# Kernel tuning notes

Hardware: AMD Instinct MI355X
Metric: run time of the kernel (lower is better)

## Reference

```python
import jax, jax.numpy as jnp
import numpy as np

B, S, H, K, V = 1024, 50, 128, 4, 100000
ROUTING_TIMES = 3

def _squash(c):
    # c: [B,K,1,H]
    cap_norm = jnp.sum(jnp.square(c), -1, keepdims=True)
    scalar_factor = cap_norm / (1.0 + cap_norm) / jnp.sqrt(cap_norm + 1e-9)
    return scalar_factor * c

def setup_inputs() -> dict:
    key = jax.random.key(0)
    k1, k2, k3, k4, k5, k6 = jax.random.split(key, 6)
    item_seq = jax.random.randint(k1, (B, S), 0, V)
    mask = jax.random.randint(k2, (B, S), 0, 2).astype(jnp.float32)
    item = jax.random.randint(k3, (B, 1), 0, V)
    emb = jax.random.normal(k4, (V, H), dtype=jnp.float32) * 0.02
    W = jax.random.normal(k5, (H, H), dtype=jnp.float32) * (1.0 / np.sqrt(H))
    # bilinear_type==0 -> capsule routing logits initialized with randn
    capsule_weight0 = jax.random.normal(k6, (B, K, S), dtype=jnp.float32)
    return {"item_seq": item_seq, "mask": mask, "item": item,
            "emb": emb, "W": W, "capsule_weight0": capsule_weight0}

def reference(item_seq, mask, item, emb, W, capsule_weight0):
    # padding_idx=0: lookups see a zeroed row 0 (and get no grad there),
    # but calculate_loss uses the raw weight matrix.
    emb_lookup = emb.at[0].set(0.0)
    seq_emb = emb_lookup[item_seq]          # [B,S,H]
    item_e = emb_lookup[item[:, 0]]         # [B,H]  (squeeze(1))

    # CapsuleNetwork, bilinear_type==0: Linear(H,H,no bias) then repeat_interleave along hidden
    h = seq_emb @ W.T                        # [B,S,H]
    hat = jnp.repeat(h, K, axis=2)           # [B,S,H*K] (repeat_interleave semantics)
    hat = hat.reshape(B, S, K, H).transpose(0, 2, 1, 3)  # [B,K,S,H]
    hat_iter = jax.lax.stop_gradient(hat)    # stop_grad=True (detach)

    atten_mask = jnp.broadcast_to(mask[:, None, :], (B, K, S))
    cw = capsule_weight0
    cap = None
    for i in range(ROUTING_TIMES):
        # torch F.softmax with no dim on a 3-D tensor uses dim=0 (batch axis) -- faithful
        sw = jax.nn.softmax(cw, axis=0)
        sw = jnp.where(atten_mask == 0, 0.0, sw)[:, :, None, :]  # [B,K,1,S]
        src = hat_iter if i < ROUTING_TIMES - 1 else hat
        cap = _squash(sw @ src)                                   # [B,K,1,H]
        if i < ROUTING_TIMES - 1:
            delta = (hat_iter @ jnp.swapaxes(cap, 3, 2)).reshape(B, K, S)
            cw = cw + delta

    user_emb = cap.reshape(B, K, H)          # multi_interest_emb

    # hard readout: pick interest with max dot against target item
    cos = jnp.einsum('bkh,bh->bk', user_emb, item_e)
    k_index = jnp.argmax(cos, axis=1)        # [B]
    best = jnp.take_along_axis(user_emb, k_index[:, None, None], axis=1)[:, 0]  # [B,H]

    # cross-entropy over all items (raw embedding weight)
    scores = best @ emb.T                    # [B,V]
    logp = jax.nn.log_softmax(scores, axis=-1)
    loss = -jnp.mean(jnp.take_along_axis(logp, item, axis=1))
    return user_emb, loss
```

## Files before the change

### kernel.cpp

```cpp
#include <hip/hip_runtime.h>
#include <math.h>

#define BB 1024
#define SS 50
#define SSP 51
#define HH 128
#define KK 4
#define VV 100000
#define NVT 782
#define NVT8 784
#define VPAD (NVT8*128)
#define KS (KK*SS)
#define NHM 400
#define NPAD_ALL 352.0f
#define CONVB 2048
#define LOG2E 1.44269504f
#define SGRID (NVT8*8)

typedef __attribute__((ext_vector_type(8))) short bf16x8;
typedef __attribute__((ext_vector_type(4))) float f32x4;

__device__ __forceinline__ ushort f2bf(float x) {
  unsigned u = __float_as_uint(x);
  unsigned r = u + 0x7FFF + ((u >> 16) & 1);
  return (ushort)(r >> 16);
}
__device__ __forceinline__ float bf2f(ushort u) {
  return __uint_as_float(((unsigned)u) << 16);
}
__device__ __forceinline__ bf16x8 cvt8(float4 a, float4 b) {
  bf16x8 r;
  r[0] = (short)f2bf(a.x); r[1] = (short)f2bf(a.y);
  r[2] = (short)f2bf(a.z); r[3] = (short)f2bf(a.w);
  r[4] = (short)f2bf(b.x); r[5] = (short)f2bf(b.y);
  r[6] = (short)f2bf(b.z); r[7] = (short)f2bf(b.w);
  return r;
}

__global__ __launch_bounds__(256) void k_pre(const float* __restrict__ emb,
                                             const float* __restrict__ cw0,
                                             float* __restrict__ cm,
                                             float* __restrict__ s1,
                                             float* __restrict__ s2,
                                             float* __restrict__ accum,
                                             const int* __restrict__ item_seq,
                                             const float* __restrict__ W,
                                             ushort* __restrict__ hb16,
                                             ushort* __restrict__ embb) {
  const int t = threadIdx.x;
  if (blockIdx.x < NHM) {
    __shared__ __align__(16) ushort sWf[32 * 512];
    const int w = t >> 6;
    const int lane = t & 63;
    const int lr = lane & 15;
    const int lq = lane >> 4;
    const int m0 = blockIdx.x * 128;

#pragma unroll
    for (int it = 0; it < 8; ++it) {
      int pos = t + it * 256;
      int ch = pos >> 6, l = pos & 63;
      int n = (ch & 7) * 16 + (l & 15);
      int k0 = (ch >> 3) * 32 + (l >> 4) * 8;
      float4 a = *(const float4*)&W[n * HH + k0];
      float4 b = *(const float4*)&W[n * HH + k0 + 4];
      *(bf16x8*)&sWf[ch * 512 + l * 8] = cvt8(a, b);
    }

    bf16x8 af[4][2];
#pragma unroll
    for (int vv = 0; vv < 2; ++vv) {
      int m = m0 + w * 32 + vv * 16 + lr;
      int idx = item_seq[m];
#pragma unroll
      for (int ks = 0; ks < 4; ++ks) {
        if (idx != 0) {
          float4 a = *(const float4*)&emb[(size_t)idx * HH + ks * 32 + lq * 8];
          float4 b = *(const float4*)&emb[(size_t)idx * HH + ks * 32 + lq * 8 + 4];
          af[ks][vv] = cvt8(a, b);
        } else {
          af[ks][vv] = (bf16x8){0, 0, 0, 0, 0, 0, 0, 0};
        }
      }
    }
    __syncthreads();

    f32x4 acc[8][2];
#pragma unroll
    for (int nt = 0; nt < 8; ++nt)
#pragma unroll
      for (int vv = 0; vv < 2; ++vv) acc[nt][vv] = (f32x4){0.f, 0.f, 0.f, 0.f};

#pragma unroll
    for (int ks = 0; ks < 4; ++ks) {
      bf16x8 bw[8];
#pragma unroll
      for (int nt = 0; nt < 8; ++nt)
        bw[nt] = *(const bf16x8*)&sWf[(ks * 8 + nt) * 512 + lane * 8];
#pragma unroll
      for (int nt = 0; nt < 8; ++nt)
#pragma unroll
        for (int vv = 0; vv < 2; ++vv)
          acc[nt][vv] = __builtin_amdgcn_mfma_f32_16x16x32_bf16(af[ks][vv], bw[nt], acc[nt][vv], 0, 0, 0);
    }

#pragma unroll
    for (int nt = 0; nt < 8; ++nt)
#pragma unroll
      for (int vv = 0; vv < 2; ++vv)
#pragma unroll
        for (int r = 0; r < 4; ++r) {
          int m = m0 + w * 32 + vv * 16 + lq * 4 + r;
          hb16[(size_t)m * HH + nt * 16 + lr] = f2bf(acc[nt][vv][r]);
        }
  } else if (blockIdx.x < NHM + KS) {
    __shared__ float red[256];
    const int c = blockIdx.x - NHM;
    if (t < 8) s1[t * KS + c] = 0.f;
    if (t >= 8 && t < 16) s2[(t - 8) * KS + c] = 0.f;
    if (c < 32) accum[c * 256 + t] = 0.f;
    float s = 0.f;
    for (int b = t; b < BB; b += 256) s += __expf(cw0[(size_t)b * KS + c]);
    red[t] = s;
    __syncthreads();
    for (int o = 128; o > 0; o >>= 1) {
      if (t < o) red[t] += red[t + o];
      __syncthreads();
    }
    if (t == 0) cm[c] = red[0];
  } else {
    const size_t stride = (size_t)CONVB * 256 * 4;
    for (size_t i = ((size_t)(blockIdx.x - NHM - KS) * 256 + t) * 4;
         i < (size_t)VPAD * HH; i += stride) {
      ushort4 o;
      if (i < (size_t)VV * HH) {
        float4 v = *(const float4*)&emb[i];
        o = make_ushort4(f2bf(v.x), f2bf(v.y), f2bf(v.z), f2bf(v.w));
      } else {
        o = make_ushort4(0, 0, 0, 0);
      }
      *(ushort4*)&embb[i] = o;
    }
  }
}

__global__ __launch_bounds__(256) void k_route(const float* __restrict__ cwsrc,
                                               float* __restrict__ cwdst,
                                               const ushort* __restrict__ hb16,
                                               const float* __restrict__ csum,
                                               int nslots,
                                               const float* __restrict__ mask,
                                               int last,
                                               float* __restrict__ out_ue,
                                               const float* __restrict__ emb,
                                               const int* __restrict__ item,
                                               ushort* __restrict__ bestb,
                                               float* __restrict__ csnext,
                                               float* __restrict__ si) {
  __shared__ ushort shT[128 * SSP];
  __shared__ float swl[KS];
  __shared__ float c32p[256];
  __shared__ float c32[128];
  __shared__ float csq[128];
  __shared__ float ie4r[32];
  __shared__ float ie4z[32];
  __shared__ float fac[4];
  __shared__ float cosk[4];
  __shared__ float cosr[4];
  __shared__ int kb;
  const int t = threadIdx.x;
  const int b = blockIdx.x;

  for (int p = t; p < (SS * HH) / 4; p += 256) {
    int flat = 4 * p;
    int s = flat >> 7, col = flat & 127;
    ushort4 v = *(const ushort4*)&hb16[(size_t)b * SS * HH + flat];
    shT[(col + 0) * SSP + s] = v.x;
    shT[(col + 1) * SSP + s] = v.y;
    shT[(col + 2) * SSP + s] = v.z;
    shT[(col + 3) * SSP + s] = v.w;
  }
  if (t < KS) {
    float den = 0.f;
    for (int g2 = 0; g2 < nslots; ++g2) den += csum[g2 * KS + t];
    float v = __expf(cwsrc[(size_t)b * KS + t]) / den;
    if (mask[b * SS + (t % SS)] == 0.0f) v = 0.0f;
    swl[t] = v;
  }
  __syncthreads();

  {
    int col = t & 127;
    int half = t >> 7;
    int k = col >> 5;
    float acc = 0.f;
    const float* swk = &swl[k * SS + half * 25];
    const ushort* hc = &shT[col * SSP + half * 25];
    for (int s = 0; s < 25; ++s) acc += swk[s] * bf2f(hc[s]);
    c32p[t] = acc;
  }
  __syncthreads();
  if (t < 128) c32[t] = c32p[t] + c32p[t + 128];
  __syncthreads();
  if (t < 4) {
    float nrm = 0.f;
#pragma unroll
    for (int j = 0; j < 32; ++j) { float c = c32[32 * t + j]; nrm += c * c; }
    nrm *= 4.0f;
    fac[t] = nrm / (1.0f + nrm) / sqrtf(nrm + 1e-9f);
  }
  __syncthreads();
  if (t < 128) csq[t] = c32[t] * fac[t >> 5];
  __syncthreads();

  if (!last) {
    if (t < KS) {
      int k = t / SS, s = t % SS;
      const float* cq = &csq[32 * k];
      float d = 0.f;
#pragma unroll
      for (int j = 0; j < 32; ++j) d += bf2f(shT[(32 * k + j) * SSP + s]) * cq[j];
      float nv = cwsrc[(size_t)b * KS + t] + 4.0f * d;
      cwdst[(size_t)b * KS + t] = nv;
      atomicAdd(&csnext[(b & 7) * KS + t], __expf(nv));
    }
  } else {
    for (int hh = t; hh < 512; hh += 256) {
      int k = hh >> 7, r = (hh & 127) >> 2;
      out_ue[(size_t)b * 512 + hh] = csq[32 * k + r];
    }
    if (t < 32) {
      int idx = item[b];
      const float* e = emb + (size_t)idx * HH + 4 * t;
      float v = e[0] + e[1] + e[2] + e[3];
      ie4r[t] = v;
      ie4z[t] = (idx == 0) ? 0.f : v;
    }
    __syncthreads();
    if (t < 4) {
      float cz = 0.f, cr = 0.f;
#pragma unroll
      for (int j = 0; j < 32; ++j) {
        cz += csq[32 * t + j] * ie4z[j];
        cr += csq[32 * t + j] * ie4r[j];
      }
      cosk[t] = cz; cosr[t] = cr;
    }
    __syncthreads();
    if (t == 0) {
      int kbest = 0; float bv = cosk[0];
#pragma unroll
      for (int k = 1; k < 4; ++k) if (cosk[k] > bv) { bv = cosk[k]; kbest = k; }
      kb = kbest;
      si[b] = cosr[kbest];
    }
    __syncthreads();
    if (t < 128) bestb[(size_t)b * HH + t] = f2bf(csq[32 * kb + (t >> 2)] * LOG2E);
  }
}

__global__ __launch_bounds__(256) void k_score_mfma(const ushort* __restrict__ bestb,
                                                    const ushort* __restrict__ embb,
                                                    float* __restrict__ accum) {
  const int lin = blockIdx.x;
  const int xcd = lin & 7;
  const int g = lin >> 3;
  const int bt8 = g & 7;
  const int vt = xcd * (NVT8 / 8) + (g >> 3);

  __shared__ __align__(16) ushort sB[32 * 512];
  float* ssmf = (float*)sB;
  const int t = threadIdx.x;
  const int w = t >> 6;
  const int lane = t & 63;
  const int lr = lane & 15;
  const int lq = lane >> 4;
  const int b0 = bt8 * 128;
  const int v0 = vt * 128 + w * 32;

  bf16x8 af[4][2];
#pragma unroll
  for (int ks = 0; ks < 4; ++ks)
#pragma unroll
    for (int vv = 0; vv < 2; ++vv)
      af[ks][vv] = *(const bf16x8*)&embb[(size_t)(v0 + vv * 16 + lr) * HH + ks * 32 + lq * 8];

#pragma unroll
  for (int it = 0; it < 8; ++it) {
    int ch = w + it * 4;
    int ks = ch >> 3, bt = ch & 7;
    const ushort* src = &bestb[(size_t)(b0 + bt * 16 + lr) * HH + ks * 32 + lq * 8];
    __builtin_amdgcn_global_load_lds(
        (const __attribute__((address_space(1))) unsigned int*)src,
        (__attribute__((address_space(3))) unsigned int*)&sB[ch * 512 + lane * 8],
        16, 0, 0);
  }

  f32x4 acc[8][2];
#pragma unroll
  for (int bt = 0; bt < 8; ++bt)
#pragma unroll
    for (int vv = 0; vv < 2; ++vv) acc[bt][vv] = (f32x4){0.f, 0.f, 0.f, 0.f};

  __syncthreads();

  bf16x8 bcur[8];
#pragma unroll
  for (int bt = 0; bt < 8; ++bt)
    bcur[bt] = *(const bf16x8*)&sB[bt * 512 + lane * 8];

#pragma unroll
  for (int ks = 0; ks < 4; ++ks) {
    bf16x8 bnxt[8];
    if (ks < 3) {
#pragma unroll
      for (int bt = 0; bt < 8; ++bt)
        bnxt[bt] = *(const bf16x8*)&sB[((ks + 1) * 8 + bt) * 512 + lane * 8];
    }
#pragma unroll
    for (int bt = 0; bt < 8; ++bt)
#pragma unroll
      for (int vv = 0; vv < 2; ++vv)
        acc[bt][vv] = __builtin_amdgcn_mfma_f32_16x16x32_bf16(af[ks][vv], bcur[bt], acc[bt][vv], 0, 0, 0);
    if (ks < 3) {
#pragma unroll
      for (int bt = 0; bt < 8; ++bt) bcur[bt] = bnxt[bt];
    }
  }

  float sacc[8];
#pragma unroll
  for (int bt = 0; bt < 8; ++bt) {
    float e[8];
#pragma unroll
    for (int vv = 0; vv < 2; ++vv)
#pragma unroll
      for (int r = 0; r < 4; ++r)
        e[vv * 4 + r] = __builtin_amdgcn_exp2f(acc[bt][vv][r]);
#pragma unroll
    for (int o = 4; o > 0; o >>= 1)
#pragma unroll
      for (int j = 0; j < 8; ++j)
        if (j < o) e[j] += e[j + o];
    float s = e[0];
    s += __shfl_xor(s, 16);
    s += __shfl_xor(s, 32);
    sacc[bt] = s;
  }

  __syncthreads();
#pragma unroll
  for (int bt = 0; bt < 8; ++bt)
    if (lq == 0) ssmf[(bt * 16 + lr) * 4 + w] = sacc[bt];
  __syncthreads();
  if (t < 128) {
    float s = ssmf[t * 4 + 0] + ssmf[t * 4 + 1] + ssmf[t * 4 + 2] + ssmf[t * 4 + 3];
    atomicAdd(&accum[(size_t)(lin & 7) * BB + b0 + t], s);
  }
}

__global__ __launch_bounds__(256) void k_loss(const float* __restrict__ accum,
                                              const float* __restrict__ si,
                                              float* __restrict__ outloss) {
  __shared__ float red[256];
  const int t = threadIdx.x;
  float s = 0.f;
  for (int b = t; b < BB; b += 256) {
    float a = 0.f;
#pragma unroll
    for (int r = 0; r < 8; ++r) a += accum[(size_t)r * BB + b];
    s += logf(a - NPAD_ALL) - si[b];
  }
  red[t] = s;
  __syncthreads();
  for (int o = 128; o > 0; o >>= 1) {
    if (t < o) red[t] += red[t + o];
    __syncthreads();
  }
  if (t == 0) outloss[0] = red[0] / (float)BB;
}

extern "C" void kernel_launch(void* const* d_in, const int* in_sizes, int n_in,
                              void* d_out, int out_size, void* d_ws, size_t ws_size,
                              hipStream_t stream) {
  const int*   item_seq = (const int*)d_in[0];
  const float* mask     = (const float*)d_in[1];
  const int*   item     = (const int*)d_in[2];
  const float* emb      = (const float*)d_in[3];
  const float* W        = (const float*)d_in[4];
  const float* cw0      = (const float*)d_in[5];
  float* out = (float*)d_out;
  float* outloss = out + (size_t)BB * KK * HH;

  float* ws = (float*)d_ws;
  float* cm    = ws;
  float* s1    = cm + 256;
  float* s2    = s1 + 8 * KS;
  float* si    = s2 + 8 * KS;
  float* accum = si + BB;
  float* cw    = accum + 8 * BB;
  ushort* hb16  = (ushort*)(cw + (size_t)BB * KS);
  ushort* embb  = hb16 + (size_t)BB * SS * HH;
  ushort* bestb = embb + (size_t)VPAD * HH;

  k_pre<<<dim3(NHM + KS + CONVB), 256, 0, stream>>>(emb, cw0, cm, s1, s2, accum,
                                                    item_seq, W, hb16, embb);

  k_route<<<dim3(BB), 256, 0, stream>>>(cw0, cw, hb16, cm, 1, mask, 0, out, emb, item, bestb, s1, si);
  k_route<<<dim3(BB), 256, 0, stream>>>(cw, cw, hb16, s1, 8, mask, 0, out, emb, item, bestb, s2, si);
  k_route<<<dim3(BB), 256, 0, stream>>>(cw, cw, hb16, s2, 8, mask, 1, out, emb, item, bestb, s1, si);

  k_score_mfma<<<dim3(SGRID), 256, 0, stream>>>(bestb, embb, accum);
  k_loss<<<dim3(1), 256, 0, stream>>>(accum, si, outloss);
}
```

Before: 197.0 us.

## Move embedding bf16 conversion into first routing launch and widen score blocks

```diff
diff --git a/kernel.cpp b/kernel.cpp
--- a/kernel.cpp
+++ b/kernel.cpp
@@ -15,7 +15,7 @@
 #define NPAD_ALL 352.0f
 #define CONVB 2048
 #define LOG2E 1.44269504f
-#define SGRID (NVT8*8)
+#define SGRID ((NVT8/2)*8)
 
 typedef __attribute__((ext_vector_type(8))) short bf16x8;
 typedef __attribute__((ext_vector_type(4))) float f32x4;
@@ -45,8 +45,7 @@
                                              float* __restrict__ accum,
                                              const int* __restrict__ item_seq,
                                              const float* __restrict__ W,
-                                             ushort* __restrict__ hb16,
-                                             ushort* __restrict__ embb) {
+                                             ushort* __restrict__ hb16) {
   const int t = threadIdx.x;
   if (blockIdx.x < NHM) {
     __shared__ __align__(16) ushort sWf[32 * 512];
@@ -113,7 +112,7 @@
           int m = m0 + w * 32 + vv * 16 + lq * 4 + r;
           hb16[(size_t)m * HH + nt * 16 + lr] = f2bf(acc[nt][vv][r]);
         }
-  } else if (blockIdx.x < NHM + KS) {
+  } else {
     __shared__ float red[256];
     const int c = blockIdx.x - NHM;
     if (t < 8) s1[t * KS + c] = 0.f;
@@ -128,19 +127,6 @@
       __syncthreads();
     }
     if (t == 0) cm[c] = red[0];
-  } else {
-    const size_t stride = (size_t)CONVB * 256 * 4;
-    for (size_t i = ((size_t)(blockIdx.x - NHM - KS) * 256 + t) * 4;
-         i < (size_t)VPAD * HH; i += stride) {
-      ushort4 o;
-      if (i < (size_t)VV * HH) {
-        float4 v = *(const float4*)&emb[i];
-        o = make_ushort4(f2bf(v.x), f2bf(v.y), f2bf(v.z), f2bf(v.w));
-      } else {
-        o = make_ushort4(0, 0, 0, 0);
-      }
-      *(ushort4*)&embb[i] = o;
-    }
   }
 }
 
@@ -156,7 +142,25 @@
                                                const int* __restrict__ item,
                                                ushort* __restrict__ bestb,
                                                float* __restrict__ csnext,
-                                               float* __restrict__ si) {
+                                               float* __restrict__ si,
+                                               ushort* __restrict__ embb) {
+  const int t = threadIdx.x;
+  if (blockIdx.x >= BB) {
+    const size_t stride = (size_t)CONVB * 256 * 4;
+    for (size_t i = ((size_t)(blockIdx.x - BB) * 256 + t) * 4;
+         i < (size_t)VPAD * HH; i += stride) {
+      ushort4 o;
+      if (i < (size_t)VV * HH) {
+        float4 v = *(const float4*)&emb[i];
+        o = make_ushort4(f2bf(v.x), f2bf(v.y), f2bf(v.z), f2bf(v.w));
+      } else {
+        o = make_ushort4(0, 0, 0, 0);
+      }
+      *(ushort4*)&embb[i] = o;
+    }
+    return;
+  }
+
   __shared__ ushort shT[128 * SSP];
   __shared__ float swl[KS];
   __shared__ float c32p[256];
@@ -168,7 +172,6 @@
   __shared__ float cosk[4];
   __shared__ float cosr[4];
   __shared__ int kb;
-  const int t = threadIdx.x;
   const int b = blockIdx.x;
 
   for (int p = t; p < (SS * HH) / 4; p += 256) {
@@ -259,24 +262,26 @@
   }
 }
 
-__global__ __launch_bounds__(256) void k_score_mfma(const ushort* __restrict__ bestb,
+__global__ __launch_bounds__(512) void k_score_mfma(const ushort* __restrict__ bestb,
                                                     const ushort* __restrict__ embb,
                                                     float* __restrict__ accum) {
   const int lin = blockIdx.x;
   const int xcd = lin & 7;
   const int g = lin >> 3;
   const int bt8 = g & 7;
-  const int vt = xcd * (NVT8 / 8) + (g >> 3);
+  const int vt0 = xcd * 98 + (g >> 3) * 2;
 
   __shared__ __align__(16) ushort sB[32 * 512];
-  float* ssmf = (float*)sB;
+  __shared__ float ssm[128][8];
   const int t = threadIdx.x;
   const int w = t >> 6;
   const int lane = t & 63;
   const int lr = lane & 15;
   const int lq = lane >> 4;
   const int b0 = bt8 * 128;
-  const int v0 = vt * 128 + w * 32;
+  const int tile = w >> 2;
+  const int ws = w & 3;
+  const int v0 = (vt0 + tile) * 128 + ws * 32;
 
   bf16x8 af[4][2];
 #pragma unroll
@@ -286,8 +291,8 @@
       af[ks][vv] = *(const bf16x8*)&embb[(size_t)(v0 + vv * 16 + lr) * HH + ks * 32 + lq * 8];
 
 #pragma unroll
-  for (int it = 0; it < 8; ++it) {
-    int ch = w + it * 4;
+  for (int it = 0; it < 4; ++it) {
+    int ch = w + it * 8;
     int ks = ch >> 3, bt = ch & 7;
     const ushort* src = &bestb[(size_t)(b0 + bt * 16 + lr) * HH + ks * 32 + lq * 8];
     __builtin_amdgcn_global_load_lds(
@@ -328,7 +333,6 @@
     }
   }
 
-  float sacc[8];
 #pragma unroll
   for (int bt = 0; bt < 8; ++bt) {
     float e[8];
@@ -345,16 +349,13 @@
     float s = e[0];
     s += __shfl_xor(s, 16);
     s += __shfl_xor(s, 32);
-    sacc[bt] = s;
-  }
-
-  __syncthreads();
-#pragma unroll
-  for (int bt = 0; bt < 8; ++bt)
-    if (lq == 0) ssmf[(bt * 16 + lr) * 4 + w] = sacc[bt];
+    if (lq == 0) ssm[bt * 16 + lr][w] = s;
+  }
   __syncthreads();
   if (t < 128) {
-    float s = ssmf[t * 4 + 0] + ssmf[t * 4 + 1] + ssmf[t * 4 + 2] + ssmf[t * 4 + 3];
+    float s = 0.f;
+#pragma unroll
+    for (int r = 0; r < 8; ++r) s += ssm[t][r];
     atomicAdd(&accum[(size_t)(lin & 7) * BB + b0 + t], s);
   }
 }
@@ -403,13 +404,13 @@
   ushort* embb  = hb16 + (size_t)BB * SS * HH;
   ushort* bestb = embb + (size_t)VPAD * HH;
 
-  k_pre<<<dim3(NHM + KS + CONVB), 256, 0, stream>>>(emb, cw0, cm, s1, s2, accum,
-                                                    item_seq, W, hb16, embb);
-
-  k_route<<<dim3(BB), 256, 0, stream>>>(cw0, cw, hb16, cm, 1, mask, 0, out, emb, item, bestb, s1, si);
-  k_route<<<dim3(BB), 256, 0, stream>>>(cw, cw, hb16, s1, 8, mask, 0, out, emb, item, bestb, s2, si);
-  k_route<<<dim3(BB), 256, 0, stream>>>(cw, cw, hb16, s2, 8, mask, 1, out, emb, item, bestb, s1, si);
-
-  k_score_mfma<<<dim3(SGRID), 256, 0, stream>>>(bestb, embb, accum);
+  k_pre<<<dim3(NHM + KS), 256, 0, stream>>>(emb, cw0, cm, s1, s2, accum,
+                                            item_seq, W, hb16);
+
+  k_route<<<dim3(BB + CONVB), 256, 0, stream>>>(cw0, cw, hb16, cm, 1, mask, 0, out, emb, item, bestb, s1, si, embb);
+  k_route<<<dim3(BB), 256, 0, stream>>>(cw, cw, hb16, s1, 8, mask, 0, out, emb, item, bestb, s2, si, embb);
+  k_route<<<dim3(BB), 256, 0, stream>>>(cw, cw, hb16, s2, 8, mask, 1, out, emb, item, bestb, s1, si, embb);
+
+  k_score_mfma<<<dim3(SGRID), 512, 0, stream>>>(bestb, embb, accum);
   k_loss<<<dim3(1), 256, 0, stream>>>(accum, si, outloss);
 }
```

Measured after the change: 189.4 us. 1.04x faster.
